# Performance work log

Measured on AMD Instinct MI355X. Metric: run time of the kernel, lower is better.

Reference implementation:

```python
import jax, jax.numpy as jnp
import numpy as np

B, S, I, H = 256, 2048, 128, 256

def setup_inputs() -> dict:
    key = jax.random.key(0)
    k1, k2, k3, k4, k5 = jax.random.split(key, 5)
    bound = 1.0 / np.sqrt(H)
    return {
        "x_in": jax.random.normal(k1, (B, S, I), dtype=jnp.float32),
        "W_ih": jax.random.uniform(k2, (H, I), jnp.float32, -bound, bound),
        "W_hh": jax.random.uniform(k3, (H, H), jnp.float32, -bound, bound),
        "b_ih": jax.random.uniform(k4, (H,), jnp.float32, -bound, bound),
        "b_hh": jax.random.uniform(k5, (H,), jnp.float32, -bound, bound),
    }

def reference(x_in, W_ih, W_hh, b_ih, b_hh):
    # batch_first=True: x_in is (B, S, I). Precompute input projection for all steps.
    # xp: (S, B, H)
    xp = jnp.einsum('bsi,hi->sbh', x_in, W_ih) + b_ih + b_hh
    h0 = jnp.zeros((x_in.shape[0], W_hh.shape[0]), dtype=x_in.dtype)

    def step(h, xp_t):
        h_new = jnp.tanh(xp_t + h @ W_hh.T)
        return h_new, h_new

    _, hs = jax.lax.scan(step, h0, xp)  # hs: (S, B, H)
    return jnp.transpose(hs, (1, 0, 2))  # (B, S, H)
```

## Files before the change

kernel.cpp:

```cpp
#include <hip/hip_runtime.h>

#define NB 256
#define NS 2048
#define NI 128
#define NH 256

typedef _Float16 h2 __attribute__((ext_vector_type(2)));
typedef _Float16 h8 __attribute__((ext_vector_type(8)));

__device__ __forceinline__ float fdot2(h2 a, h2 b, float c) {
#if defined(__has_builtin)
#if __has_builtin(__builtin_amdgcn_fdot2)
  return __builtin_amdgcn_fdot2(a, b, c, false);
#else
  return c + (float)a[0] * (float)b[0] + (float)a[1] * (float)b[1];
#endif
#else
  return c + (float)a[0] * (float)b[0] + (float)a[1] * (float)b[1];
#endif
}

__global__ __launch_bounds__(1024, 4) void elman_splitk(
    const float* __restrict__ x_in,
    const float* __restrict__ W_ih,
    const float* __restrict__ W_hh,
    const float* __restrict__ b_ih,
    const float* __restrict__ b_hh,
    float* __restrict__ out)
{
  const int b   = blockIdx.x;
  const int tid = threadIdx.x;
  const int o   = tid >> 2;
  const int q   = tid & 3;

  __shared__ __align__(16) _Float16 h_sm[4 * 72];
  __shared__ __align__(16) _Float16 x_sm[2][4 * 40];

  h2 whh[32];
  {
    const float4* wr = (const float4*)(W_hh + (size_t)o * NH + q * 64);
#pragma unroll
    for (int k = 0; k < 16; ++k) {
      float4 w = wr[k];
      whh[2 * k]     = h2{(_Float16)w.x, (_Float16)w.y};
      whh[2 * k + 1] = h2{(_Float16)w.z, (_Float16)w.w};
    }
  }
  h2 wih[16];
  {
    const float4* wr = (const float4*)(W_ih + (size_t)o * NI + q * 32);
#pragma unroll
    for (int k = 0; k < 8; ++k) {
      float4 w = wr[k];
      wih[2 * k]     = h2{(_Float16)w.x, (_Float16)w.y};
      wih[2 * k + 1] = h2{(_Float16)w.z, (_Float16)w.w};
    }
  }
  const float bias = b_ih[o] + b_hh[o];

  if (q == 0) h_sm[(o >> 6) * 72 + (o & 63)] = (_Float16)0.f;
  const float* xrow = x_in + (size_t)b * NS * NI;
  float xn = 0.f;
  if (tid < NI) {
    x_sm[0][(tid >> 5) * 40 + (tid & 31)] = (_Float16)xrow[tid];
    xn = xrow[NI + tid];
  }
  __syncthreads();

  float* orow = out + (size_t)b * NS * NH;

  for (int s = 0; s < NS; ++s) {
    const h8* hp = (const h8*)(h_sm + q * 72);
    const h8* xp = (const h8*)(x_sm[s & 1] + q * 40);

    float a0 = 0.f, a1 = 0.f, a2 = 0.f, a3 = 0.f;
#pragma unroll
    for (int k = 0; k < 8; ++k) {
      h8 v = hp[k];
      a0 = fdot2(whh[4 * k + 0], __builtin_shufflevector(v, v, 0, 1), a0);
      a1 = fdot2(whh[4 * k + 1], __builtin_shufflevector(v, v, 2, 3), a1);
      a2 = fdot2(whh[4 * k + 2], __builtin_shufflevector(v, v, 4, 5), a2);
      a3 = fdot2(whh[4 * k + 3], __builtin_shufflevector(v, v, 6, 7), a3);
    }
#pragma unroll
    for (int k = 0; k < 4; ++k) {
      h8 v = xp[k];
      a0 = fdot2(wih[4 * k + 0], __builtin_shufflevector(v, v, 0, 1), a0);
      a1 = fdot2(wih[4 * k + 1], __builtin_shufflevector(v, v, 2, 3), a1);
      a2 = fdot2(wih[4 * k + 2], __builtin_shufflevector(v, v, 4, 5), a2);
      a3 = fdot2(wih[4 * k + 3], __builtin_shufflevector(v, v, 6, 7), a3);
    }
    float r = (a0 + a1) + (a2 + a3);
    r += __shfl_xor(r, 1);
    r += __shfl_xor(r, 2);
    float z = bias + r;

    float zc = fminf(fmaxf(z, -30.f), 30.f);
    float e = __expf(2.f * zc);
    float hnew = (e - 1.f) / (e + 1.f);

    if (q == 0) orow[(size_t)s * NH + o] = hnew;

    __syncthreads();
    if (q == 0) h_sm[(o >> 6) * 72 + (o & 63)] = (_Float16)hnew;
    if (tid < NI) x_sm[(s + 1) & 1][(tid >> 5) * 40 + (tid & 31)] = (_Float16)xn;
    __syncthreads();

    if (tid < NI) {
      int sn = (s + 2 < NS) ? (s + 2) : (NS - 1);
      xn = xrow[(size_t)sn * NI + tid];
    }
  }
}

extern "C" void kernel_launch(void* const* d_in, const int* in_sizes, int n_in,
                              void* d_out, int out_size, void* d_ws, size_t ws_size,
                              hipStream_t stream) {
  const float* x_in = (const float*)d_in[0];
  const float* W_ih = (const float*)d_in[1];
  const float* W_hh = (const float*)d_in[2];
  const float* b_ih = (const float*)d_in[3];
  const float* b_hh = (const float*)d_in[4];
  float* out = (float*)d_out;

  elman_splitk<<<NB, 1024, 0, stream>>>(x_in, W_ih, W_hh, b_ih, b_hh, out);
}
```

Measured before the change: 2.265 ms.

## Compute recurrent matvec with MFMA 16x16x32 f16 instead of packed fdot2

Replaces the per-thread fdot2 split-K dot products with MFMA instructions. The hidden state and input are packed into one shared vector, broadcast as the A operand (every row of the 16-row tile is the same vector), and W_hh/W_ih are held as register-resident B fragments, with 8 waves of 512 threads each covering 32 outputs. The aim is to cut the ALU instruction count and the shuffle reductions on the serial per-step critical path. In exchange, 15 of the 16 MFMA rows are wasted, and the x prefetch distance drops from two steps to one, so more load latency may be exposed.

New measurement: 2.201 ms. 2.8% less time.

```diff
diff --git a/kernel.cpp b/kernel.cpp
--- a/kernel.cpp
+++ b/kernel.cpp
@@ -4,23 +4,14 @@
 #define NS 2048
 #define NI 128
 #define NH 256
+#define KTOT (NH + NI)
+#define NKT (KTOT / 32)
+#define NTPW 2
 
-typedef _Float16 h2 __attribute__((ext_vector_type(2)));
-typedef _Float16 h8 __attribute__((ext_vector_type(8)));
+typedef _Float16 h8v __attribute__((ext_vector_type(8)));
+typedef float f4v __attribute__((ext_vector_type(4)));
 
-__device__ __forceinline__ float fdot2(h2 a, h2 b, float c) {
-#if defined(__has_builtin)
-#if __has_builtin(__builtin_amdgcn_fdot2)
-  return __builtin_amdgcn_fdot2(a, b, c, false);
-#else
-  return c + (float)a[0] * (float)b[0] + (float)a[1] * (float)b[1];
-#endif
-#else
-  return c + (float)a[0] * (float)b[0] + (float)a[1] * (float)b[1];
-#endif
-}
-
-__global__ __launch_bounds__(1024, 4) void elman_splitk(
+__global__ __launch_bounds__(512, 2) void elman_mfma(
     const float* __restrict__ x_in,
     const float* __restrict__ W_ih,
     const float* __restrict__ W_hh,
@@ -28,88 +19,83 @@
     const float* __restrict__ b_hh,
     float* __restrict__ out)
 {
-  const int b   = blockIdx.x;
-  const int tid = threadIdx.x;
-  const int o   = tid >> 2;
-  const int q   = tid & 3;
+  const int b    = blockIdx.x;
+  const int tid  = threadIdx.x;
+  const int wave = tid >> 6;
+  const int lane = tid & 63;
+  const int g    = lane >> 4;
+  const int c    = lane & 15;
 
-  __shared__ __align__(16) _Float16 h_sm[4 * 72];
-  __shared__ __align__(16) _Float16 x_sm[2][4 * 40];
+  __shared__ __align__(16) _Float16 A_sm[KTOT];
 
-  h2 whh[32];
-  {
-    const float4* wr = (const float4*)(W_hh + (size_t)o * NH + q * 64);
+  const int n0 = (wave * NTPW + 0) * 16 + c;
+  const int n1 = (wave * NTPW + 1) * 16 + c;
+
+  h8v Bf0[NKT], Bf1[NKT];
 #pragma unroll
-    for (int k = 0; k < 16; ++k) {
-      float4 w = wr[k];
-      whh[2 * k]     = h2{(_Float16)w.x, (_Float16)w.y};
-      whh[2 * k + 1] = h2{(_Float16)w.z, (_Float16)w.w};
-    }
+  for (int kt = 0; kt < NKT; ++kt) {
+    const int k = kt * 32 + g * 8;
+    const float* s0 = (k < NH) ? (W_hh + (size_t)n0 * NH + k)
+                               : (W_ih + (size_t)n0 * NI + (k - NH));
+    const float* s1 = (k < NH) ? (W_hh + (size_t)n1 * NH + k)
+                               : (W_ih + (size_t)n1 * NI + (k - NH));
+    h8v v0, v1;
+#pragma unroll
+    for (int j = 0; j < 8; ++j) { v0[j] = (_Float16)s0[j]; v1[j] = (_Float16)s1[j]; }
+    Bf0[kt] = v0;
+    Bf1[kt] = v1;
   }
-  h2 wih[16];
-  {
-    const float4* wr = (const float4*)(W_ih + (size_t)o * NI + q * 32);
-#pragma unroll
-    for (int k = 0; k < 8; ++k) {
-      float4 w = wr[k];
-      wih[2 * k]     = h2{(_Float16)w.x, (_Float16)w.y};
-      wih[2 * k + 1] = h2{(_Float16)w.z, (_Float16)w.w};
-    }
-  }
-  const float bias = b_ih[o] + b_hh[o];
+  const float bias0 = b_ih[n0] + b_hh[n0];
+  const float bias1 = b_ih[n1] + b_hh[n1];
 
-  if (q == 0) h_sm[(o >> 6) * 72 + (o & 63)] = (_Float16)0.f;
+  if (tid < NH) A_sm[tid] = (_Float16)0.f;
   const float* xrow = x_in + (size_t)b * NS * NI;
-  float xn = 0.f;
-  if (tid < NI) {
-    x_sm[0][(tid >> 5) * 40 + (tid & 31)] = (_Float16)xrow[tid];
-    xn = xrow[NI + tid];
-  }
+  if (tid < NI) A_sm[NH + tid] = (_Float16)xrow[tid];
   __syncthreads();
 
   float* orow = out + (size_t)b * NS * NH;
 
   for (int s = 0; s < NS; ++s) {
-    const h8* hp = (const h8*)(h_sm + q * 72);
-    const h8* xp = (const h8*)(x_sm[s & 1] + q * 40);
+    h8v a[NKT];
+#pragma unroll
+    for (int kt = 0; kt < NKT; ++kt)
+      a[kt] = *(const h8v*)(A_sm + kt * 32 + g * 8);
 
-    float a0 = 0.f, a1 = 0.f, a2 = 0.f, a3 = 0.f;
+    float xn = 0.f;
+    if (tid < NI) {
+      int sn = (s + 1 < NS) ? (s + 1) : s;
+      xn = xrow[(size_t)sn * NI + tid];
+    }
+
+    f4v acc0 = {0.f, 0.f, 0.f, 0.f};
+    f4v acc1 = {0.f, 0.f, 0.f, 0.f};
 #pragma unroll
-    for (int k = 0; k < 8; ++k) {
-      h8 v = hp[k];
-      a0 = fdot2(whh[4 * k + 0], __builtin_shufflevector(v, v, 0, 1), a0);
-      a1 = fdot2(whh[4 * k + 1], __builtin_shufflevector(v, v, 2, 3), a1);
-      a2 = fdot2(whh[4 * k + 2], __builtin_shufflevector(v, v, 4, 5), a2);
-      a3 = fdot2(whh[4 * k + 3], __builtin_shufflevector(v, v, 6, 7), a3);
+    for (int kt = 0; kt < NKT; ++kt) {
+      acc0 = __builtin_amdgcn_mfma_f32_16x16x32_f16(a[kt], Bf0[kt], acc0, 0, 0, 0);
+      acc1 = __builtin_amdgcn_mfma_f32_16x16x32_f16(a[kt], Bf1[kt], acc1, 0, 0, 0);
     }
-#pragma unroll
-    for (int k = 0; k < 4; ++k) {
-      h8 v = xp[k];
-      a0 = fdot2(wih[4 * k + 0], __builtin_shufflevector(v, v, 0, 1), a0);
-      a1 = fdot2(wih[4 * k + 1], __builtin_shufflevector(v, v, 2, 3), a1);
-      a2 = fdot2(wih[4 * k + 2], __builtin_shufflevector(v, v, 4, 5), a2);
-      a3 = fdot2(wih[4 * k + 3], __builtin_shufflevector(v, v, 6, 7), a3);
+
+    float h0 = 0.f, h1 = 0.f;
+    if (lane < 16) {
+      float z0 = bias0 + acc0[0];
+      float z1 = bias1 + acc1[0];
+      z0 = fminf(fmaxf(z0, -30.f), 30.f);
+      z1 = fminf(fmaxf(z1, -30.f), 30.f);
+      float e0 = __expf(2.f * z0);
+      float e1 = __expf(2.f * z1);
+      h0 = (e0 - 1.f) / (e0 + 1.f);
+      h1 = (e1 - 1.f) / (e1 + 1.f);
+      orow[(size_t)s * NH + n0] = h0;
+      orow[(size_t)s * NH + n1] = h1;
     }
-    float r = (a0 + a1) + (a2 + a3);
-    r += __shfl_xor(r, 1);
-    r += __shfl_xor(r, 2);
-    float z = bias + r;
-
-    float zc = fminf(fmaxf(z, -30.f), 30.f);
-    float e = __expf(2.f * zc);
-    float hnew = (e - 1.f) / (e + 1.f);
-
-    if (q == 0) orow[(size_t)s * NH + o] = hnew;
 
     __syncthreads();
-    if (q == 0) h_sm[(o >> 6) * 72 + (o & 63)] = (_Float16)hnew;
-    if (tid < NI) x_sm[(s + 1) & 1][(tid >> 5) * 40 + (tid & 31)] = (_Float16)xn;
+    if (lane < 16) {
+      A_sm[n0] = (_Float16)h0;
+      A_sm[n1] = (_Float16)h1;
+    }
+    if (tid < NI) A_sm[NH + tid] = (_Float16)xn;
     __syncthreads();
-
-    if (tid < NI) {
-      int sn = (s + 2 < NS) ? (s + 2) : (NS - 1);
-      xn = xrow[(size_t)sn * NI + tid];
-    }
   }
 }
 
@@ -123,5 +109,5 @@
   const float* b_hh = (const float*)d_in[4];
   float* out = (float*)d_out;
 
-  elman_splitk<<<NB, 1024, 0, stream>>>(x_in, W_ih, W_hh, b_ih, b_hh, out);
+  elman_mfma<<<NB, 512, 0, stream>>>(x_in, W_ih, W_hh, b_ih, b_hh, out);
 }
```
